# Kernel optimization log

Measured on AMD Instinct MI355X. Metric: run time of the kernel, lower is better.

## Reference

```python
import jax, jax.numpy as jnp
import numpy as np

D_MODEL = 1024
NHEAD = 16
D_HEAD = D_MODEL // NHEAD
D_FF = 4096
B, S = 2, 2048
EPS = 1e-5


def _linear_params(key, d_in, d_out):
    kw, kb = jax.random.split(key)
    bound = 1.0 / np.sqrt(d_in)
    W = jax.random.uniform(kw, (d_out, d_in), jnp.float32, -bound, bound)
    b = jax.random.uniform(kb, (d_out,), jnp.float32, -bound, bound)
    return W, b


def setup_inputs() -> dict:
    key = jax.random.key(0)
    ks = jax.random.split(key, 8)
    x = jax.random.normal(ks[0], (B, S, D_MODEL), jnp.float32)
    Wq, bq = _linear_params(ks[1], D_MODEL, D_MODEL)
    Wk, bk = _linear_params(ks[2], D_MODEL, D_MODEL)
    Wv, bv = _linear_params(ks[3], D_MODEL, D_MODEL)
    Wo, bo = _linear_params(ks[4], D_MODEL, D_MODEL)
    W1, b1 = _linear_params(ks[5], D_MODEL, D_FF)
    W2, b2 = _linear_params(ks[6], D_FF, D_MODEL)
    g1 = jnp.ones((D_MODEL,), jnp.float32); be1 = jnp.zeros((D_MODEL,), jnp.float32)
    g2 = jnp.ones((D_MODEL,), jnp.float32); be2 = jnp.zeros((D_MODEL,), jnp.float32)
    return dict(x=x, Wq=Wq, bq=bq, Wk=Wk, bk=bk, Wv=Wv, bv=bv, Wo=Wo, bo=bo,
                W1=W1, b1=b1, W2=W2, b2=b2, g1=g1, be1=be1, g2=g2, be2=be2)


def _layernorm(x, g, b):
    mu = jnp.mean(x, axis=-1, keepdims=True)
    var = jnp.mean(jnp.square(x - mu), axis=-1, keepdims=True)
    return (x - mu) * jax.lax.rsqrt(var + EPS) * g + b


def reference(x, Wq, bq, Wk, bk, Wv, bv, Wo, bo, W1, b1, W2, b2, g1, be1, g2, be2):
    b_, s_, _ = x.shape
    # QKV projections (nn.Linear: x @ W.T + b)
    q = x @ Wq.T + bq
    k = x @ Wk.T + bk
    v = x @ Wv.T + bv
    # split heads -> [b, h, s, d_head]
    qh = q.reshape(b_, s_, NHEAD, D_HEAD).transpose(0, 2, 1, 3)
    kh = k.reshape(b_, s_, NHEAD, D_HEAD).transpose(0, 2, 1, 3)
    vh = v.reshape(b_, s_, NHEAD, D_HEAD).transpose(0, 2, 1, 3)
    scores = jnp.einsum('bhqd,bhkd->bhqk', qh, kh) / jnp.sqrt(jnp.float32(D_HEAD))
    attn_w = jax.nn.softmax(scores, axis=-1)
    attn_out = jnp.einsum('bhqk,bhkd->bhqd', attn_w, vh)
    attn_concat = attn_out.transpose(0, 2, 1, 3).reshape(b_, s_, D_MODEL)
    attn_proj = attn_concat @ Wo.T + bo
    # residual + LN1
    h = _layernorm(x + attn_proj, g1, be1)
    # FFN
    ffn = jax.nn.relu(h @ W1.T + b1) @ W2.T + b2
    # residual + LN2
    return _layernorm(h + ffn, g2, be2)
```

## Files before the change

### kernel.cpp

```cpp
#include <hip/hip_runtime.h>
#include <hip/hip_bf16.h>

#define D_MODEL 1024
#define NHEAD 16
#define D_HEAD 64
#define D_FF 4096
#define BATCH 2
#define SEQ 2048
#define M_TOK (BATCH * SEQ)
#define EPS 1e-5f
#define QKV_N 3072

using bf16 = __hip_bfloat16;
typedef __attribute__((ext_vector_type(8))) short short8;
typedef __attribute__((ext_vector_type(4))) short short4v;
typedef __attribute__((ext_vector_type(4))) float float4v;
typedef __attribute__((ext_vector_type(16))) float float16v;

__device__ __forceinline__ float b2f(unsigned short u) {
    union { unsigned int i; float f; } v; v.i = ((unsigned int)u) << 16; return v.f;
}
__device__ __forceinline__ unsigned short f2b(float f) {
    union { float f; unsigned int u; } v; v.f = f;
    unsigned int r = v.u + 0x7FFFu + ((v.u >> 16) & 1u);
    return (unsigned short)(r >> 16);
}
__device__ __forceinline__ float loadAt(const void* p, size_t i, int f32) {
    if (f32) return ((const float*)p)[i];
    return b2f(((const unsigned short*)p)[i]);
}
__device__ __forceinline__ void async16(const void* g, void* lds) {
    __builtin_amdgcn_global_load_lds(
        (const __attribute__((address_space(1))) unsigned int*)g,
        (__attribute__((address_space(3))) unsigned int*)lds, 16, 0, 0);
}
__device__ __forceinline__ unsigned int cvt_pk_bf16(float lo, float hi) {
    unsigned int r;
    asm("v_cvt_pk_bf16_f32 %0, %1, %2" : "=v"(r) : "v"(lo), "v"(hi));
    return r;
}
__device__ __forceinline__ void pl32_swap(unsigned int& a, unsigned int& b) {
    asm("v_permlane32_swap_b32 %0, %1" : "+v"(a), "+v"(b));
}

__global__ void detect_kernel(const unsigned short* __restrict__ x, int* __restrict__ flag) {
    __shared__ int cnt;
    if (threadIdx.x == 0) cnt = 0;
    __syncthreads();
    int c = 0;
    for (int i = threadIdx.x; i < 8192; i += 256) {
        unsigned short u = x[i];
        int e = (u >> 7) & 0xFF;
        if (e >= 0xF0) c++;
    }
    atomicAdd(&cnt, c);
    __syncthreads();
    if (threadIdx.x == 0) { flag[0] = (cnt > 16) ? 1 : 0; flag[1] = 0; }
}

__global__ __launch_bounds__(256) void cast_bf16_kernel(
    const void* __restrict__ src, bf16* __restrict__ dst, int n,
    const int* __restrict__ flagp) {
    const int f32 = *flagp;
    int i0 = (blockIdx.x * 256 + threadIdx.x) * 8;
    if (i0 >= n) return;
    short8 v;
    if (f32) {
        const float* pf = (const float*)src + i0;
        float4v f0 = *(const float4v*)pf;
        float4v f1 = *(const float4v*)(pf + 4);
#pragma unroll
        for (int i = 0; i < 4; i++) { v[i] = (short)f2b(f0[i]); v[4 + i] = (short)f2b(f1[i]); }
    } else {
        v = *(const short8*)((const short*)src + i0);
    }
    *(short8*)((short*)dst + i0) = v;
}

__global__ __launch_bounds__(256) void cast3_bf16_kernel(
    const void* __restrict__ s0, const void* __restrict__ s1,
    const void* __restrict__ s2, bf16* __restrict__ dst,
    const int* __restrict__ flagp) {
    const int f32 = *flagp;
    int i0 = (blockIdx.x * 256 + threadIdx.x) * 8;
    const int part = i0 >> 20;
    const int off = i0 & ((1 << 20) - 1);
    const void* src = (part == 0) ? s0 : (part == 1) ? s1 : s2;
    short8 v;
    if (f32) {
        const float* pf = (const float*)src + off;
        float4v f0 = *(const float4v*)pf;
        float4v f1 = *(const float4v*)(pf + 4);
#pragma unroll
        for (int i = 0; i < 4; i++) { v[i] = (short)f2b(f0[i]); v[4 + i] = (short)f2b(f1[i]); }
    } else {
        v = *(const short8*)((const short*)src + off);
    }
    *(short8*)((short*)dst + i0) = v;
}

__global__ __launch_bounds__(256) void cast2_bf16_kernel(
    const void* __restrict__ s0, const void* __restrict__ s1,
    bf16* __restrict__ d0, bf16* __restrict__ d1,
    const int* __restrict__ flagp) {
    const int f32 = *flagp;
    int i0 = (blockIdx.x * 256 + threadIdx.x) * 8;
    const void* src; short* dst; int off;
    if (i0 < (1 << 20)) { src = s0; dst = (short*)d0; off = i0; }
    else                { src = s1; dst = (short*)d1; off = i0 - (1 << 20); }
    short8 v;
    if (f32) {
        const float* pf = (const float*)src + off;
        float4v f0 = *(const float4v*)pf;
        float4v f1 = *(const float4v*)(pf + 4);
#pragma unroll
        for (int i = 0; i < 4; i++) { v[i] = (short)f2b(f0[i]); v[4 + i] = (short)f2b(f1[i]); }
    } else {
        v = *(const short8*)((const short*)src + off);
    }
    *(short8*)(dst + off) = v;
}

__device__ __forceinline__ void stage8(const void* src, size_t off, int f32, short* dst) {
    short8 v;
    if (f32) {
        const float* pf = (const float*)src + off;
        float4v f0 = *(const float4v*)pf;
        float4v f1 = *(const float4v*)(pf + 4);
#pragma unroll
        for (int i = 0; i < 4; i++) { v[i] = (short)f2b(f0[i]); v[4 + i] = (short)f2b(f1[i]); }
    } else {
        v = *(const short8*)((const short*)src + off);
    }
    *(short8*)dst = v;
}

template <int MF, int NF, bool RELU, bool BDYN>
__global__ __launch_bounds__(256) void gemm_mfma(
    const bf16* __restrict__ A, const void* __restrict__ B,
    const void* __restrict__ bias0, const void* __restrict__ bias1,
    const void* __restrict__ bias2, int nb1, int nb2,
    bf16* __restrict__ C, int N, int K, const int* __restrict__ inFlagp) {
    constexpr int BM = 32 * MF, BN = 32 * NF;
    __shared__ short As[BM * 64];
    __shared__ short Bs[BN * 64];
    const int tid = threadIdx.x;
    const int lane = tid & 63;
    const int wv = tid >> 6;
    const int wm = wv & 1, wn = wv >> 1;
    const int quad = lane >> 4, lrow = lane & 15;
    const int rowM = blockIdx.y * BM;
    const int rowN = blockIdx.x * BN;
    const int inf = *inFlagp;

    float4v acc[MF][NF];
    const float4v zero = {0.f, 0.f, 0.f, 0.f};
#pragma unroll
    for (int i = 0; i < MF; i++)
#pragma unroll
        for (int j = 0; j < NF; j++) acc[i][j] = zero;

    const int sRow = lane >> 3;
    const int gChunk = (lane & 7) ^ sRow;

    for (int k0 = 0; k0 < K; k0 += 64) {
#pragma unroll
        for (int rd = 0; rd < MF; rd++) {
            const short* gp = (const short*)A +
                (size_t)(rowM + rd * 32 + wv * 8 + sRow) * K + k0 + gChunk * 8;
            async16(gp, &As[rd * 2048 + wv * 512]);
        }
        if (!BDYN) {
#pragma unroll
            for (int rd = 0; rd < NF; rd++) {
                const short* gp = (const short*)B +
                    (size_t)(rowN + rd * 32 + wv * 8 + sRow) * K + k0 + gChunk * 8;
                async16(gp, &Bs[rd * 2048 + wv * 512]);
            }
        } else {
            const int brow = tid >> 2;
            const int c0 = (tid & 3) * 2;
#pragma unroll
            for (int cc = 0; cc < 2; cc++) {
                int slot = c0 + cc;
                int g = slot ^ (brow & 7);
                stage8(B, (size_t)(rowN + brow) * K + k0 + g * 8, inf,
                       &Bs[brow * 64 + slot * 8]);
            }
        }
        __syncthreads();
#pragma unroll
        for (int ks = 0; ks < 2; ks++) {
            short8 a_frag[MF], b_frag[NF];
#pragma unroll
            for (int i = 0; i < MF; i++) {
                const int row = wm * MF * 16 + i * 16 + lrow;
                const int slot = (ks * 4 + quad) ^ (row & 7);
                a_frag[i] = *(const short8*)&As[row * 64 + slot * 8];
            }
#pragma unroll
            for (int j = 0; j < NF; j++) {
                const int row = wn * NF * 16 + j * 16 + lrow;
                const int slot = (ks * 4 + quad) ^ (row & 7);
                b_frag[j] = *(const short8*)&Bs[row * 64 + slot * 8];
            }
#pragma unroll
            for (int i = 0; i < MF; i++)
#pragma unroll
                for (int j = 0; j < NF; j++)
                    acc[i][j] = __builtin_amdgcn_mfma_f32_16x16x32_bf16(
                        a_frag[i], b_frag[j], acc[i][j], 0, 0, 0);
        }
        __syncthreads();
    }

    const int mB = rowM + wm * MF * 16, nB = rowN + wn * NF * 16;
    unsigned short* Cu = (unsigned short*)C;
#pragma unroll
    for (int j = 0; j < NF; j++) {
        const int col = nB + j * 16 + lrow;
        float bv;
        if (col < nb1)      bv = loadAt(bias0, col, inf);
        else if (col < nb2) bv = loadAt(bias1, col - nb1, inf);
        else                bv = loadAt(bias2, col - nb2, inf);
#pragma unroll
        for (int i = 0; i < MF; i++) {
#pragma unroll
            for (int r = 0; r < 4; r++) {
                const int rowg = mB + i * 16 + quad * 4 + r;
                float vv = acc[i][j][r] + bv;
                if (RELU) vv = fmaxf(vv, 0.0f);
                Cu[(size_t)rowg * N + col] = f2b(vv);
            }
        }
    }
}

#define FSTRIDE 66
__global__ __launch_bounds__(256) void flash_attn_kernel(
    const bf16* __restrict__ Qb, const bf16* __restrict__ Kb,
    const bf16* __restrict__ Vb, bf16* __restrict__ O) {
    const int bid = blockIdx.x;
    const int qt = bid & 15;
    const int h  = (bid >> 4) & 15;
    const int b  = bid >> 8;
    const int q0 = qt * 128;
    const int tid = threadIdx.x;
    const int lane = tid & 63;
    const int wv = tid >> 6;
    const int half = lane >> 5;
    const int l31 = lane & 31;

    __shared__ short Ab[128 * FSTRIDE];
    __shared__ short Ks[2][64 * 64];
    __shared__ short Vt[2][64 * FSTRIDE];

    const size_t headOff = (size_t)h * D_HEAD;
    const float SCF = 0.18033688f;

    {
        int r = tid >> 1, c0 = (tid & 1) * 32;
        const short* src = (const short*)Qb + (size_t)(b * SEQ + q0 + r) * QKV_N + headOff + c0;
#pragma unroll
        for (int ch = 0; ch < 4; ch++) {
            short8 v = *(const short8*)(src + ch * 8);
            short8 o;
#pragma unroll
            for (int e = 0; e < 8; e++)
                o[e] = (short)f2b(b2f((unsigned short)v[e]) * SCF);
            *(short8*)&Ab[r * FSTRIDE + c0 + ch * 8] = o;
        }
    }

    const int sRow = lane >> 3;
    const int gChunk = (lane & 7) ^ sRow;
    const int vjp = (tid & 31) * 2;
    const int vd0 = (tid >> 5) * 8;

#pragma unroll
    for (int rd = 0; rd < 2; rd++) {
        const short* gp = (const short*)Kb +
            (size_t)(b * SEQ + rd * 32 + wv * 8 + sRow) * QKV_N + headOff + gChunk * 8;
        async16(gp, &Ks[0][(rd * 32 + wv * 8) * 64]);
    }
    short8 v0, v1;
    {
        const short* s0 = (const short*)Vb + (size_t)(b * SEQ + vjp) * QKV_N + headOff + vd0;
        v0 = *(const short8*)s0;
        v1 = *(const short8*)(s0 + QKV_N);
    }
    __syncthreads();

    short8 a_q[4];
#pragma unroll
    for (int ks = 0; ks < 4; ks++)
        a_q[ks] = *(const short8*)&Ab[(wv * 32 + l31) * FSTRIDE + ks * 16 + half * 8];

#pragma unroll
    for (int e = 0; e < 8; e++) {
        unsigned int wa = (unsigned int)(unsigned short)v0[e] |
                          ((unsigned int)(unsigned short)v1[e] << 16);
        *(unsigned int*)&Vt[0][(vd0 + e) * FSTRIDE + vjp] = wa;
    }
    __syncthreads();

    float16v o_acc[2];
#pragma unroll
    for (int i = 0; i < 16; i++) { o_acc[0][i] = 0.f; o_acc[1][i] = 0.f; }
    float lsum = 0.f;

    int cb = 0;
    for (int t = 0; t < SEQ / 64; t++) {
        const int jn = (t < SEQ / 64 - 1) ? (t + 1) * 64 : t * 64;
#pragma unroll
        for (int rd = 0; rd < 2; rd++) {
            const short* gp = (const short*)Kb +
                (size_t)(b * SEQ + jn + rd * 32 + wv * 8 + sRow) * QKV_N + headOff + gChunk * 8;
            async16(gp, &Ks[cb ^ 1][(rd * 32 + wv * 8) * 64]);
        }
        {
            const short* s0 = (const short*)Vb + (size_t)(b * SEQ + jn + vjp) * QKV_N + headOff + vd0;
            v0 = *(const short8*)s0;
            v1 = *(const short8*)(s0 + QKV_N);
        }

        float16v s_acc[2];
#pragma unroll
        for (int i = 0; i < 16; i++) { s_acc[0][i] = 0.f; s_acc[1][i] = 0.f; }
        __builtin_amdgcn_s_setprio(1);
#pragma unroll
        for (int ks = 0; ks < 4; ks++)
#pragma unroll
            for (int jb = 0; jb < 2; jb++) {
                const int row = jb * 32 + l31;
                const int slot = (ks * 2 + half) ^ (l31 & 7);
                short8 kfr = *(const short8*)&Ks[cb][row * 64 + slot * 8];
                s_acc[jb] = __builtin_amdgcn_mfma_f32_32x32x16_bf16(kfr, a_q[ks], s_acc[jb], 0, 0, 0);
            }
        __builtin_amdgcn_s_setprio(0);

#pragma unroll
        for (int jb = 0; jb < 2; jb++)
#pragma unroll
            for (int reg = 0; reg < 16; reg++) {
                float pv = exp2f(s_acc[jb][reg]);
                s_acc[jb][reg] = pv;
                lsum += pv;
            }

        short8 pa[4];
#pragma unroll
        for (int jb = 0; jb < 2; jb++)
#pragma unroll
            for (int c = 0; c < 2; c++) {
                unsigned int a0 = cvt_pk_bf16(s_acc[jb][8 * c + 0], s_acc[jb][8 * c + 1]);
                unsigned int a1 = cvt_pk_bf16(s_acc[jb][8 * c + 2], s_acc[jb][8 * c + 3]);
                unsigned int b0 = cvt_pk_bf16(s_acc[jb][8 * c + 4], s_acc[jb][8 * c + 5]);
                unsigned int b1 = cvt_pk_bf16(s_acc[jb][8 * c + 6], s_acc[jb][8 * c + 7]);
                pl32_swap(a0, b0);
                pl32_swap(a1, b1);
                union { unsigned int w[4]; short8 s; } u;
                u.w[0] = a0; u.w[1] = a1; u.w[2] = b0; u.w[3] = b1;
                pa[jb * 2 + c] = u.s;
            }

        __builtin_amdgcn_s_setprio(1);
#pragma unroll
        for (int ks = 0; ks < 4; ks++) {
#pragma unroll
            for (int db = 0; db < 2; db++) {
                short8 vbf = *(const short8*)&Vt[cb][(db * 32 + l31) * FSTRIDE + ks * 16 + half * 8];
                o_acc[db] = __builtin_amdgcn_mfma_f32_32x32x16_bf16(pa[ks], vbf, o_acc[db], 0, 0, 0);
            }
        }
        __builtin_amdgcn_s_setprio(0);

#pragma unroll
        for (int e = 0; e < 8; e++) {
            unsigned int wa = (unsigned int)(unsigned short)v0[e] |
                              ((unsigned int)(unsigned short)v1[e] << 16);
            *(unsigned int*)&Vt[cb ^ 1][(vd0 + e) * FSTRIDE + vjp] = wa;
        }
        __syncthreads();
        cb ^= 1;
    }

    const float ltot = lsum + __shfl_xor(lsum, 32);
    unsigned short* Ou = (unsigned short*)O;
#pragma unroll
    for (int reg = 0; reg < 16; reg++) {
        const int rowC = (reg & 3) + 8 * (reg >> 2) + 4 * half;
        const float invl = 1.0f / __shfl(ltot, rowC);
        const int rowg = b * SEQ + q0 + wv * 32 + rowC;
#pragma unroll
        for (int db = 0; db < 2; db++)
            Ou[(size_t)rowg * D_MODEL + headOff + db * 32 + l31] =
                f2b(o_acc[db][reg] * invl);
    }
}

template <bool OUT_F32>
__global__ __launch_bounds__(256) void add_ln_kernel(
    const void* __restrict__ X, const bf16* __restrict__ R,
    const void* __restrict__ g, const void* __restrict__ be,
    void* __restrict__ Y,
    const int* __restrict__ xFlagp, const int* __restrict__ wFlagp) {
    const int xf = *xFlagp;
    const int wf = *wFlagp;
    const int row = blockIdx.x;
    const size_t base = (size_t)row * D_MODEL;
    const int tid = threadIdx.x;
    const int i0 = tid * 4;
    __shared__ float red[256];
    float v[4];
    if (xf) {
        float4v xv = *(const float4v*)((const float*)X + base + i0);
        short4v rv = *(const short4v*)((const short*)R + base + i0);
#pragma unroll
        for (int i = 0; i < 4; i++) v[i] = xv[i] + b2f((unsigned short)rv[i]);
    } else {
        short4v xv = *(const short4v*)((const short*)X + base + i0);
        short4v rv = *(const short4v*)((const short*)R + base + i0);
#pragma unroll
        for (int i = 0; i < 4; i++) v[i] = b2f((unsigned short)xv[i]) + b2f((unsigned short)rv[i]);
    }
    float s = v[0] + v[1] + v[2] + v[3];
    red[tid] = s; __syncthreads();
    for (int s2 = 128; s2 > 0; s2 >>= 1) {
        if (tid < s2) red[tid] += red[tid + s2];
        __syncthreads();
    }
    float mu = red[0] * (1.0f / D_MODEL);
    __syncthreads();
    float s2v = 0.f;
#pragma unroll
    for (int i = 0; i < 4; i++) { float dd = v[i] - mu; s2v += dd * dd; }
    red[tid] = s2v; __syncthreads();
    for (int s2 = 128; s2 > 0; s2 >>= 1) {
        if (tid < s2) red[tid] += red[tid + s2];
        __syncthreads();
    }
    float rstd = rsqrtf(red[0] * (1.0f / D_MODEL) + EPS);
    float gv[4], bv[4];
    if (wf) {
        float4v gg = *(const float4v*)((const float*)g + i0);
        float4v bb = *(const float4v*)((const float*)be + i0);
#pragma unroll
        for (int i = 0; i < 4; i++) { gv[i] = gg[i]; bv[i] = bb[i]; }
    } else {
        short4v gg = *(const short4v*)((const short*)g + i0);
        short4v bb = *(const short4v*)((const short*)be + i0);
#pragma unroll
        for (int i = 0; i < 4; i++) { gv[i] = b2f((unsigned short)gg[i]); bv[i] = b2f((unsigned short)bb[i]); }
    }
    if (OUT_F32) {
        float4v o;
#pragma unroll
        for (int i = 0; i < 4; i++) o[i] = (v[i] - mu) * rstd * gv[i] + bv[i];
        *(float4v*)((float*)Y + base + i0) = o;
    } else {
        short4v o;
#pragma unroll
        for (int i = 0; i < 4; i++) o[i] = (short)f2b((v[i] - mu) * rstd * gv[i] + bv[i]);
        *(short4v*)((short*)Y + base + i0) = o;
    }
}

extern "C" void kernel_launch(void* const* d_in, const int* in_sizes, int n_in,
                              void* d_out, int out_size, void* d_ws, size_t ws_size,
                              hipStream_t stream) {
    const void* x  = d_in[0];
    const void* Wq = d_in[1];  const void* bq = d_in[2];
    const void* Wk = d_in[3];  const void* bk = d_in[4];
    const void* Wv = d_in[5];  const void* bv = d_in[6];
    const void* Wo = d_in[7];  const void* bo = d_in[8];
    const void* W1 = d_in[9];  const void* b1 = d_in[10];
    const void* W2 = d_in[11]; const void* b2 = d_in[12];
    const void* g1 = d_in[13]; const void* be1 = d_in[14];
    const void* g2 = d_in[15]; const void* be2 = d_in[16];

    char* ws = (char*)d_ws;
    const size_t MB = 1024 * 1024;
    bf16* xb     = (bf16*)(ws + 0 * MB);
    bf16* wqkvb  = (bf16*)(ws + 8 * MB);
    bf16* wob    = (bf16*)(ws + 14 * MB);
    bf16* qkv    = (bf16*)(ws + 16 * MB);
    bf16* concat = (bf16*)(ws + 40 * MB);
    bf16* w1b    = (bf16*)(ws + 0 * MB);
    bf16* proj   = (bf16*)(ws + 16 * MB);
    bf16* hb     = (bf16*)(ws + 8 * MB);
    bf16* ffn1   = (bf16*)(ws + 16 * MB);
    bf16* ffn2   = (bf16*)(ws + 0 * MB);
    const bool castW2 = (ws_size >= 56 * MB + 8);
    bf16* w2b    = (bf16*)(ws + 48 * MB);
    int*  flag   = (int*)(ws + (castW2 ? 56 * MB : 48 * MB));

    const int* fIn = flag;
    const int* fBf = flag + 1;

    dim3 blk(256);

    detect_kernel<<<dim3(1), blk, 0, stream>>>((const unsigned short*)x, flag);
    cast_bf16_kernel<<<dim3((M_TOK * D_MODEL / 8 + 255) / 256), blk, 0, stream>>>(x, xb, M_TOK * D_MODEL, fIn);
    cast3_bf16_kernel<<<dim3(3 * D_MODEL * D_MODEL / 8 / 256), blk, 0, stream>>>(Wq, Wk, Wv, wqkvb, fIn);
    if (castW2)
        cast_bf16_kernel<<<dim3((D_FF * D_MODEL / 8 + 255) / 256), blk, 0, stream>>>(W2, w2b, D_FF * D_MODEL, fIn);
    gemm_mfma<4, 4, false, false><<<dim3(QKV_N / 128, M_TOK / 128), blk, 0, stream>>>(
        xb, wqkvb, bq, bk, bv, 1024, 2048, qkv, QKV_N, D_MODEL, fIn);
    cast2_bf16_kernel<<<dim3(5 * D_MODEL * D_MODEL / 8 / 256), blk, 0, stream>>>(Wo, W1, wob, w1b, fIn);
    flash_attn_kernel<<<dim3(BATCH * NHEAD * (SEQ / 128)), dim3(256), 0, stream>>>(
        qkv, qkv + D_MODEL, qkv + 2 * D_MODEL, concat);
    gemm_mfma<2, 2, false, false><<<dim3(D_MODEL / 64, M_TOK / 64), blk, 0, stream>>>(
        concat, wob, bo, bo, bo, D_MODEL, D_MODEL, proj, D_MODEL, D_MODEL, fIn);
    add_ln_kernel<false><<<dim3(M_TOK), blk, 0, stream>>>(x, proj, g1, be1, hb, fIn, fIn);
    gemm_mfma<4, 4, true, false><<<dim3(D_FF / 128, M_TOK / 128), blk, 0, stream>>>(
        hb, w1b, b1, b1, b1, D_FF, D_FF, ffn1, D_FF, D_MODEL, fIn);
    if (castW2)
        gemm_mfma<2, 2, false, false><<<dim3(D_MODEL / 64, M_TOK / 64), blk, 0, stream>>>(
            ffn1, w2b, b2, b2, b2, D_MODEL, D_MODEL, ffn2, D_MODEL, D_FF, fIn);
    else
        gemm_mfma<2, 2, false, true><<<dim3(D_MODEL / 64, M_TOK / 64), blk, 0, stream>>>(
            ffn1, W2, b2, b2, b2, D_MODEL, D_MODEL, ffn2, D_MODEL, D_FF, fIn);
    add_ln_kernel<true><<<dim3(M_TOK), blk, 0, stream>>>(hb, ffn2, g2, be2, d_out, fBf, fIn);
}
```

Baseline: 383.5 us.

## Double-buffer shared-memory tiles in small GEMMs to overlap loads with MFMA

Adds a PIPE template option to the MFMA GEMM that keeps two LDS buffers for the A and B tiles. The next K-tile is issued into the alternate buffer before computing the current one, leaving one barrier per step instead of two. It is enabled for the 64x64-tile output-projection and FFN2 GEMMs, aiming to hide global-load latency behind compute. In exchange it doubles LDS use for those kernels and issues one redundant reload of the last tile.

```diff
diff --git a/kernel.cpp b/kernel.cpp
--- a/kernel.cpp
+++ b/kernel.cpp
@@ -135,15 +135,17 @@
     *(short8*)dst = v;
 }
 
-template <int MF, int NF, bool RELU, bool BDYN>
+template <int MF, int NF, bool RELU, bool BDYN, bool PIPE>
 __global__ __launch_bounds__(256) void gemm_mfma(
     const bf16* __restrict__ A, const void* __restrict__ B,
     const void* __restrict__ bias0, const void* __restrict__ bias1,
     const void* __restrict__ bias2, int nb1, int nb2,
     bf16* __restrict__ C, int N, int K, const int* __restrict__ inFlagp) {
+    static_assert(!BDYN || NF == 2, "BDYN staging layout assumes BN=64");
     constexpr int BM = 32 * MF, BN = 32 * NF;
-    __shared__ short As[BM * 64];
-    __shared__ short Bs[BN * 64];
+    constexpr int NB = PIPE ? 2 : 1;
+    __shared__ short As[NB][BM * 64];
+    __shared__ short Bs[NB][BN * 64];
     const int tid = threadIdx.x;
     const int lane = tid & 63;
     const int wv = tid >> 6;
@@ -163,19 +165,19 @@
     const int sRow = lane >> 3;
     const int gChunk = (lane & 7) ^ sRow;
 
-    for (int k0 = 0; k0 < K; k0 += 64) {
+    auto stage = [&](int bi, int k0) {
 #pragma unroll
         for (int rd = 0; rd < MF; rd++) {
             const short* gp = (const short*)A +
                 (size_t)(rowM + rd * 32 + wv * 8 + sRow) * K + k0 + gChunk * 8;
-            async16(gp, &As[rd * 2048 + wv * 512]);
+            async16(gp, &As[bi][rd * 2048 + wv * 512]);
         }
         if (!BDYN) {
 #pragma unroll
             for (int rd = 0; rd < NF; rd++) {
                 const short* gp = (const short*)B +
                     (size_t)(rowN + rd * 32 + wv * 8 + sRow) * K + k0 + gChunk * 8;
-                async16(gp, &Bs[rd * 2048 + wv * 512]);
+                async16(gp, &Bs[bi][rd * 2048 + wv * 512]);
             }
         } else {
             const int brow = tid >> 2;
@@ -185,10 +187,12 @@
                 int slot = c0 + cc;
                 int g = slot ^ (brow & 7);
                 stage8(B, (size_t)(rowN + brow) * K + k0 + g * 8, inf,
-                       &Bs[brow * 64 + slot * 8]);
-            }
-        }
-        __syncthreads();
+                       &Bs[bi][brow * 64 + slot * 8]);
+            }
+        }
+    };
+
+    auto compute = [&](int bi) {
 #pragma unroll
         for (int ks = 0; ks < 2; ks++) {
             short8 a_frag[MF], b_frag[NF];
@@ -196,13 +200,13 @@
             for (int i = 0; i < MF; i++) {
                 const int row = wm * MF * 16 + i * 16 + lrow;
                 const int slot = (ks * 4 + quad) ^ (row & 7);
-                a_frag[i] = *(const short8*)&As[row * 64 + slot * 8];
+                a_frag[i] = *(const short8*)&As[bi][row * 64 + slot * 8];
             }
 #pragma unroll
             for (int j = 0; j < NF; j++) {
                 const int row = wn * NF * 16 + j * 16 + lrow;
                 const int slot = (ks * 4 + quad) ^ (row & 7);
-                b_frag[j] = *(const short8*)&Bs[row * 64 + slot * 8];
+                b_frag[j] = *(const short8*)&Bs[bi][row * 64 + slot * 8];
             }
 #pragma unroll
             for (int i = 0; i < MF; i++)
@@ -211,7 +215,27 @@
                     acc[i][j] = __builtin_amdgcn_mfma_f32_16x16x32_bf16(
                         a_frag[i], b_frag[j], acc[i][j], 0, 0, 0);
         }
+    };
+
+    if (PIPE) {
+        stage(0, 0);
         __syncthreads();
+        const int NSTEP = K / 64;
+        int bi = 0;
+        for (int s = 0; s < NSTEP; s++) {
+            const int kn = ((s + 1 < NSTEP) ? (s + 1) : s) * 64;
+            stage(bi ^ 1, kn);
+            compute(bi);
+            __syncthreads();
+            bi ^= 1;
+        }
+    } else {
+        for (int k0 = 0; k0 < K; k0 += 64) {
+            stage(0, k0);
+            __syncthreads();
+            compute(0);
+            __syncthreads();
+        }
     }
 
     const int mB = rowM + wm * MF * 16, nB = rowN + wn * NF * 16;
@@ -505,21 +529,21 @@
     cast3_bf16_kernel<<<dim3(3 * D_MODEL * D_MODEL / 8 / 256), blk, 0, stream>>>(Wq, Wk, Wv, wqkvb, fIn);
     if (castW2)
         cast_bf16_kernel<<<dim3((D_FF * D_MODEL / 8 + 255) / 256), blk, 0, stream>>>(W2, w2b, D_FF * D_MODEL, fIn);
-    gemm_mfma<4, 4, false, false><<<dim3(QKV_N / 128, M_TOK / 128), blk, 0, stream>>>(
+    gemm_mfma<4, 4, false, false, false><<<dim3(QKV_N / 128, M_TOK / 128), blk, 0, stream>>>(
         xb, wqkvb, bq, bk, bv, 1024, 2048, qkv, QKV_N, D_MODEL, fIn);
     cast2_bf16_kernel<<<dim3(5 * D_MODEL * D_MODEL / 8 / 256), blk, 0, stream>>>(Wo, W1, wob, w1b, fIn);
     flash_attn_kernel<<<dim3(BATCH * NHEAD * (SEQ / 128)), dim3(256), 0, stream>>>(
         qkv, qkv + D_MODEL, qkv + 2 * D_MODEL, concat);
-    gemm_mfma<2, 2, false, false><<<dim3(D_MODEL / 64, M_TOK / 64), blk, 0, stream>>>(
+    gemm_mfma<2, 2, false, false, true><<<dim3(D_MODEL / 64, M_TOK / 64), blk, 0, stream>>>(
         concat, wob, bo, bo, bo, D_MODEL, D_MODEL, proj, D_MODEL, D_MODEL, fIn);
     add_ln_kernel<false><<<dim3(M_TOK), blk, 0, stream>>>(x, proj, g1, be1, hb, fIn, fIn);
-    gemm_mfma<4, 4, true, false><<<dim3(D_FF / 128, M_TOK / 128), blk, 0, stream>>>(
+    gemm_mfma<4, 4, true, false, false><<<dim3(D_FF / 128, M_TOK / 128), blk, 0, stream>>>(
         hb, w1b, b1, b1, b1, D_FF, D_FF, ffn1, D_FF, D_MODEL, fIn);
     if (castW2)
-        gemm_mfma<2, 2, false, false><<<dim3(D_MODEL / 64, M_TOK / 64), blk, 0, stream>>>(
+        gemm_mfma<2, 2, false, false, true><<<dim3(D_MODEL / 64, M_TOK / 64), blk, 0, stream>>>(
             ffn1, w2b, b2, b2, b2, D_MODEL, D_MODEL, ffn2, D_MODEL, D_FF, fIn);
     else
-        gemm_mfma<2, 2, false, true><<<dim3(D_MODEL / 64, M_TOK / 64), blk, 0, stream>>>(
+        gemm_mfma<2, 2, false, true, true><<<dim3(D_MODEL / 64, M_TOK / 64), blk, 0, stream>>>(
             ffn1, W2, b2, b2, b2, D_MODEL, D_MODEL, ffn2, D_MODEL, D_FF, fIn);
     add_ln_kernel<true><<<dim3(M_TOK), blk, 0, stream>>>(hb, ffn2, g2, be2, d_out, fBf, fIn);
 }
```

New measurement: 390.7 us. No clear change (+1.9%).
